# Kernel optimization log

Measured on AMD Instinct MI355X. Metric: run time of the kernel, lower is better.

## Reference

```python
import jax, jax.numpy as jnp
import numpy as np

L, H, NH, I = 12, 768, 12, 3072
DH = H // NH
EPS = 1e-12
STD = 0.02

def _ln(x, g, b):
    m = jnp.mean(x, axis=-1, keepdims=True)
    v = jnp.mean(jnp.square(x - m), axis=-1, keepdims=True)
    return (x - m) * jax.lax.rsqrt(v + EPS) * g + b

def setup_inputs() -> dict:
    key = jax.random.key(0)
    ks = jax.random.split(key, 6)
    return {
        "hidden_states": jax.random.normal(ks[0], (8, 512, H), dtype=jnp.float32),
        "attention_mask": jnp.zeros((8, 1, 1, 512), dtype=jnp.float32),
        "normA_gamma": jnp.ones((L, H), jnp.float32),
        "normA_beta": jnp.zeros((L, H), jnp.float32),
        "normB_gamma": jnp.ones((L, H), jnp.float32),
        "normB_beta": jnp.zeros((L, H), jnp.float32),
        "wa": jax.random.normal(ks[1], (L, 3 * H, H), jnp.float32) * STD,
        "ba": jnp.zeros((L, 3 * H), jnp.float32),
        "wb": jax.random.normal(ks[2], (L, H, H), jnp.float32) * STD,
        "bb": jnp.zeros((L, H), jnp.float32),
        "wc": jax.random.normal(ks[3], (L, I, H), jnp.float32) * STD,
        "bc": jnp.zeros((L, I), jnp.float32),
        "wd": jax.random.normal(ks[4], (L, H, I), jnp.float32) * STD,
        "bd": jnp.zeros((L, H), jnp.float32),
    }

def _encoder(hidden_states, attention_mask, normA_gamma, normA_beta, normB_gamma,
             normB_beta, wa, ba, wb, bb, wc, bc, wd, bd):
    B, S, _ = hidden_states.shape
    scale = 1.0 / jnp.sqrt(jnp.float32(DH))

    def layer(x, p):
        ga, bA, gB, bB_, Wa, Ba, Wb, Bb, Wc, Bc, Wd, Bd = p
        # fused QKV: [B,S,3H]
        qkv = jnp.einsum('bsh,oh->bso', x, Wa) + Ba
        q, k, v = jnp.split(qkv, 3, axis=-1)
        q = q.reshape(B, S, NH, DH)
        k = k.reshape(B, S, NH, DH)
        v = v.reshape(B, S, NH, DH)
        scores = jnp.einsum('bqnd,bknd->bnqk', q, k) * scale + attention_mask
        probs = jax.nn.softmax(scores, axis=-1)
        ctx = jnp.einsum('bnqk,bknd->bqnd', probs, v).reshape(B, S, H)
        attn_out = jnp.einsum('bsh,oh->bso', ctx, Wb) + Bb
        x = _ln(x + attn_out, ga, bA)           # post-LN after attention
        h = jax.nn.gelu(jnp.einsum('bsh,ih->bsi', x, Wc) + Bc, approximate=False)
        ffn_out = jnp.einsum('bsi,hi->bsh', h, Wd) + Bd
        x = _ln(x + ffn_out, gB, bB_)           # post-LN after FFN
        return x, None

    params = (normA_gamma, normA_beta, normB_gamma, normB_beta,
              wa, ba, wb, bb, wc, bc, wd, bd)
    out, _ = jax.lax.scan(layer, hidden_states, params)
    return out

def reference(hidden_states, attention_mask, normA_gamma, normA_beta, normB_gamma,
              normB_beta, wa, ba, wb, bb, wc, bc, wd, bd):
    return _encoder(hidden_states, attention_mask, normA_gamma, normA_beta,
                    normB_gamma, normB_beta, wa, ba, wb, bb, wc, bc, wd, bd)
```

## Files before the change

kernel.cpp:

```cpp
#include <hip/hip_runtime.h>
#include <hip/hip_bf16.h>
#include <cmath>

typedef __bf16 bf16;
typedef __attribute__((ext_vector_type(8))) __bf16 bf16x8;
typedef __attribute__((ext_vector_type(4))) float f32x4;

#define DEV __device__ __forceinline__

constexpr int HDIM = 768, NHEADS = 12, DHEAD = 64, IDIM = 3072, BATCH = 8, SEQ = 512;
constexpr int MTOK = BATCH * SEQ;
constexpr int H3 = 3 * HDIM;
constexpr float SCALE = 0.125f;

DEV void gld16(const bf16* g, bf16* l) {
  __builtin_amdgcn_global_load_lds((const __attribute__((address_space(1))) void*)g,
                                   (__attribute__((address_space(3))) void*)l, 16, 0, 0);
}

__global__ void k_cvt_all(const float* __restrict__ a, const float* __restrict__ b,
                          const float* __restrict__ c, const float* __restrict__ d,
                          bf16* __restrict__ oa, bf16* __restrict__ ob,
                          bf16* __restrict__ oc, bf16* __restrict__ od,
                          long na, long nb, long nc, long nd) {
  long i0 = ((long)blockIdx.x * blockDim.x + threadIdx.x) * 4;
  long st = (long)gridDim.x * blockDim.x * 4;
  union U { bf16 t[4]; short4 s; };
  for (long i = i0; i < na; i += st) {
    float4 v = *(const float4*)(a + i);
    U u; u.t[0] = (bf16)v.x; u.t[1] = (bf16)v.y; u.t[2] = (bf16)v.z; u.t[3] = (bf16)v.w;
    *(short4*)(oa + i) = u.s;
  }
  for (long i = i0; i < nb; i += st) {
    float4 v = *(const float4*)(b + i);
    U u; u.t[0] = (bf16)v.x; u.t[1] = (bf16)v.y; u.t[2] = (bf16)v.z; u.t[3] = (bf16)v.w;
    *(short4*)(ob + i) = u.s;
  }
  for (long i = i0; i < nc; i += st) {
    float4 v = *(const float4*)(c + i);
    U u; u.t[0] = (bf16)v.x; u.t[1] = (bf16)v.y; u.t[2] = (bf16)v.z; u.t[3] = (bf16)v.w;
    *(short4*)(oc + i) = u.s;
  }
  for (long i = i0; i < nd; i += st) {
    float4 v = *(const float4*)(d + i);
    U u; u.t[0] = (bf16)v.x; u.t[1] = (bf16)v.y; u.t[2] = (bf16)v.z; u.t[3] = (bf16)v.w;
    *(short4*)(od + i) = u.s;
  }
}

__global__ void k_initx(const float* __restrict__ s, float* __restrict__ xf,
                        bf16* __restrict__ xb, int n4) {
  int i = blockIdx.x * blockDim.x + threadIdx.x;
  int st = gridDim.x * blockDim.x;
  for (; i < n4; i += st) {
    float4 v = ((const float4*)s)[i];
    ((float4*)xf)[i] = v;
    union { bf16 t[4]; short4 q; } u;
    u.t[0] = (bf16)v.x; u.t[1] = (bf16)v.y; u.t[2] = (bf16)v.z; u.t[3] = (bf16)v.w;
    ((short4*)xb)[i] = u.q;
  }
}

template <int OUT>
__global__ __launch_bounds__(256) void k_gemm(const bf16* __restrict__ A,
                                              const bf16* __restrict__ W,
                                              const float* __restrict__ bias,
                                              void* __restrict__ C,
                                              bf16* __restrict__ vt,
                                              int M, int N, int K) {
  __shared__ alignas(128) bf16 As[2][128 * 32];
  __shared__ alignas(128) bf16 Bs[2][128 * 32];
  const int tid = threadIdx.x;
  const int lane = tid & 63, wave = tid >> 6;
  const int wr = wave >> 1, wc = wave & 1;
  const int bx = blockIdx.x, by = blockIdx.y;
  const bf16* Ab = A + (size_t)by * 128 * K;
  const bf16* Bb = W + (size_t)bx * 128 * K;
  const int s0 = tid, s1 = tid + 256;
  const int r0 = s0 >> 2, c0 = ((s0 & 3) ^ ((r0 >> 1) & 3)) << 3;
  const int r1 = s1 >> 2, c1 = ((s1 & 3) ^ ((r1 >> 1) & 3)) << 3;

  f32x4 acc[4][4] = {};
  const int KT = K >> 5;
  int cur = 0;
  gld16(Ab + (size_t)r0 * K + c0, &As[0][s0 * 8]);
  gld16(Ab + (size_t)r1 * K + c1, &As[0][s1 * 8]);
  gld16(Bb + (size_t)r0 * K + c0, &Bs[0][s0 * 8]);
  gld16(Bb + (size_t)r1 * K + c1, &Bs[0][s1 * 8]);

  const int r = lane & 15, kg = lane >> 4;
  for (int kt = 0; kt < KT; ++kt) {
    __syncthreads();
    if (kt + 1 < KT) {
      int k0 = (kt + 1) << 5;
      gld16(Ab + (size_t)r0 * K + k0 + c0, &As[cur ^ 1][s0 * 8]);
      gld16(Ab + (size_t)r1 * K + k0 + c1, &As[cur ^ 1][s1 * 8]);
      gld16(Bb + (size_t)r0 * K + k0 + c0, &Bs[cur ^ 1][s0 * 8]);
      gld16(Bb + (size_t)r1 * K + k0 + c1, &Bs[cur ^ 1][s1 * 8]);
    }
    const bf16* Ac = As[cur];
    const bf16* Bc = Bs[cur];
    bf16x8 af[4], bfr[4];
#pragma unroll
    for (int m = 0; m < 4; ++m) {
      int row = wr * 64 + m * 16 + r;
      af[m] = *(const bf16x8*)(Ac + row * 32 + ((kg ^ ((row >> 1) & 3)) << 3));
    }
#pragma unroll
    for (int n = 0; n < 4; ++n) {
      int row = wc * 64 + n * 16 + r;
      bfr[n] = *(const bf16x8*)(Bc + row * 32 + ((kg ^ ((row >> 1) & 3)) << 3));
    }
#pragma unroll
    for (int m = 0; m < 4; ++m)
#pragma unroll
      for (int n = 0; n < 4; ++n)
        acc[m][n] = __builtin_amdgcn_mfma_f32_16x16x32_bf16(af[m], bfr[n], acc[m][n], 0, 0, 0);
    cur ^= 1;
  }
  const int g = lane >> 4, c16 = lane & 15;
#pragma unroll
  for (int m = 0; m < 4; ++m) {
#pragma unroll
    for (int n = 0; n < 4; ++n) {
      int col = bx * 128 + wc * 64 + n * 16 + c16;
      float bv = bias[col];
      if (OUT == 3 && col >= 2 * HDIM) {
        int hh = (col - 2 * HDIM) >> 6, dd = (col - 2 * HDIM) & 63;
        int row0 = by * 128 + wr * 64 + m * 16 + g * 4;
        int bb_ = row0 >> 9, ss = row0 & 511;
        union { bf16 t[4]; short4 q; } u;
#pragma unroll
        for (int j = 0; j < 4; ++j) u.t[j] = (bf16)(acc[m][n][j] + bv);
        *(short4*)(vt + (((size_t)(bb_ * NHEADS + hh) * DHEAD + dd) * SEQ + ss)) = u.q;
      } else {
#pragma unroll
        for (int j = 0; j < 4; ++j) {
          int row = by * 128 + wr * 64 + m * 16 + g * 4 + j;
          float v = acc[m][n][j] + bv;
          if (OUT == 2) v = 0.5f * v * (1.0f + erff(v * 0.70710678118f));
          ((bf16*)C)[(size_t)row * N + col] = (bf16)v;
        }
      }
    }
  }
}

__global__ __launch_bounds__(256) void k_gemm_sk(const bf16* __restrict__ A,
                                                 const bf16* __restrict__ W,
                                                 bf16* __restrict__ C,
                                                 int M, int N, int Kc, int ld) {
  __shared__ alignas(128) bf16 As[2][128 * 32];
  __shared__ alignas(128) bf16 Bs[2][128 * 32];
  const int tid = threadIdx.x;
  const int lane = tid & 63, wave = tid >> 6;
  const int wr = wave >> 1, wc = wave & 1;
  const int bx = blockIdx.x, by = blockIdx.y, kz = blockIdx.z;
  const bf16* Ab = A + (size_t)by * 128 * ld + (size_t)kz * Kc;
  const bf16* Bb = W + (size_t)bx * 128 * ld + (size_t)kz * Kc;
  bf16* Cz = C + (size_t)kz * M * N;
  const int s0 = tid, s1 = tid + 256;
  const int r0 = s0 >> 2, c0 = ((s0 & 3) ^ ((r0 >> 1) & 3)) << 3;
  const int r1 = s1 >> 2, c1 = ((s1 & 3) ^ ((r1 >> 1) & 3)) << 3;

  f32x4 acc[4][4] = {};
  const int KT = Kc >> 5;
  int cur = 0;
  gld16(Ab + (size_t)r0 * ld + c0, &As[0][s0 * 8]);
  gld16(Ab + (size_t)r1 * ld + c1, &As[0][s1 * 8]);
  gld16(Bb + (size_t)r0 * ld + c0, &Bs[0][s0 * 8]);
  gld16(Bb + (size_t)r1 * ld + c1, &Bs[0][s1 * 8]);

  const int r = lane & 15, kg = lane >> 4;
  for (int kt = 0; kt < KT; ++kt) {
    __syncthreads();
    if (kt + 1 < KT) {
      int k0 = (kt + 1) << 5;
      gld16(Ab + (size_t)r0 * ld + k0 + c0, &As[cur ^ 1][s0 * 8]);
      gld16(Ab + (size_t)r1 * ld + k0 + c1, &As[cur ^ 1][s1 * 8]);
      gld16(Bb + (size_t)r0 * ld + k0 + c0, &Bs[cur ^ 1][s0 * 8]);
      gld16(Bb + (size_t)r1 * ld + k0 + c1, &Bs[cur ^ 1][s1 * 8]);
    }
    const bf16* Ac = As[cur];
    const bf16* Bc = Bs[cur];
    bf16x8 af[4], bfr[4];
#pragma unroll
    for (int m = 0; m < 4; ++m) {
      int row = wr * 64 + m * 16 + r;
      af[m] = *(const bf16x8*)(Ac + row * 32 + ((kg ^ ((row >> 1) & 3)) << 3));
    }
#pragma unroll
    for (int n = 0; n < 4; ++n) {
      int row = wc * 64 + n * 16 + r;
      bfr[n] = *(const bf16x8*)(Bc + row * 32 + ((kg ^ ((row >> 1) & 3)) << 3));
    }
#pragma unroll
    for (int m = 0; m < 4; ++m)
#pragma unroll
      for (int n = 0; n < 4; ++n)
        acc[m][n] = __builtin_amdgcn_mfma_f32_16x16x32_bf16(af[m], bfr[n], acc[m][n], 0, 0, 0);
    cur ^= 1;
  }
  const int g = lane >> 4, c16 = lane & 15;
#pragma unroll
  for (int m = 0; m < 4; ++m)
#pragma unroll
    for (int n = 0; n < 4; ++n) {
      int col = bx * 128 + wc * 64 + n * 16 + c16;
#pragma unroll
      for (int j = 0; j < 4; ++j) {
        int row = by * 128 + wr * 64 + m * 16 + g * 4 + j;
        Cz[(size_t)row * N + col] = (bf16)acc[m][n][j];
      }
    }
}

__global__ __launch_bounds__(256) void k_attn(const bf16* __restrict__ qkv,
                                              const bf16* __restrict__ vT,
                                              const float* __restrict__ mask,
                                              bf16* __restrict__ ctx) {
  __shared__ alignas(128) bf16 smem[20480];
  bf16* Qs = smem;
  bf16* Ks = smem + 4096;
  bf16* Vs = smem;
  bf16* Ps = smem + 16384;
  const int tid = threadIdx.x, lane = tid & 63, wave = tid >> 6;
  const int q0 = blockIdx.x * 64;
  const int h = blockIdx.y, b = blockIdx.z;
  const int bh = b * NHEADS + h;
  const bf16* qbase = qkv + (size_t)(b * SEQ) * H3 + h * DHEAD;
  const bf16* kbase = qbase + HDIM;
  const bf16* Vsrc = vT + (size_t)bh * DHEAD * SEQ;
  const int r15 = lane & 15, kg = lane >> 4;

  for (int s = tid; s < 512; s += 256) {
    int r = s >> 3, sl = s & 7;
    gld16(qbase + (size_t)(q0 + r) * H3 + ((sl ^ (r & 7)) << 3), &Qs[s * 8]);
  }
  f32x4 acc[32];
#pragma unroll
  for (int f = 0; f < 32; ++f) acc[f] = (f32x4){0.f, 0.f, 0.f, 0.f};

  for (int half = 0; half < 2; ++half) {
    for (int s = tid; s < 2048; s += 256) {
      int r = s >> 3, sl = s & 7;
      gld16(kbase + (size_t)(half * 256 + r) * H3 + ((sl ^ (r & 7)) << 3), &Ks[s * 8]);
    }
    __syncthreads();
#pragma unroll
    for (int ks = 0; ks < 2; ++ks) {
      int qrow = wave * 16 + r15;
      int sl = ks * 4 + kg;
      bf16x8 aq = *(const bf16x8*)(Qs + qrow * 64 + ((sl ^ (qrow & 7)) << 3));
#pragma unroll
      for (int nf = 0; nf < 16; ++nf) {
        int krow = nf * 16 + r15;
        bf16x8 bk = *(const bf16x8*)(Ks + krow * 64 + ((sl ^ (krow & 7)) << 3));
        acc[half * 16 + nf] =
            __builtin_amdgcn_mfma_f32_16x16x32_bf16(aq, bk, acc[half * 16 + nf], 0, 0, 0);
      }
    }
    __syncthreads();
  }

#pragma unroll
  for (int i = 0; i < 8; ++i) {
    int g16 = tid + i * 256;
    int d = g16 >> 5, c = g16 & 31;
    gld16(Vsrc + (size_t)d * SEQ + ((c ^ (d & 7)) << 3), &Vs[g16 * 8]);
  }

  const float* mrow = mask + b * SEQ;
#pragma unroll
  for (int f = 0; f < 32; ++f) {
    float mv = mrow[f * 16 + r15];
#pragma unroll
    for (int j = 0; j < 4; ++j) acc[f][j] = acc[f][j] * SCALE + mv;
  }
#pragma unroll
  for (int j = 0; j < 4; ++j) {
    float m = -1e30f;
#pragma unroll
    for (int f = 0; f < 32; ++f) m = fmaxf(m, acc[f][j]);
    m = fmaxf(m, __shfl_xor(m, 1));
    m = fmaxf(m, __shfl_xor(m, 2));
    m = fmaxf(m, __shfl_xor(m, 4));
    m = fmaxf(m, __shfl_xor(m, 8));
    float sum = 0.f;
#pragma unroll
    for (int f = 0; f < 32; ++f) { acc[f][j] = __expf(acc[f][j] - m); sum += acc[f][j]; }
    sum += __shfl_xor(sum, 1);
    sum += __shfl_xor(sum, 2);
    sum += __shfl_xor(sum, 4);
    sum += __shfl_xor(sum, 8);
    float inv = 1.0f / sum;
#pragma unroll
    for (int f = 0; f < 32; ++f) acc[f][j] *= inv;
  }
  __syncthreads();

  f32x4 pvacc[4] = {};
  bf16* Pw = Ps + wave * (16 * 32);
#pragma unroll
  for (int half = 0; half < 2; ++half) {
    if (half == 1) {
      __syncthreads();
#pragma unroll
      for (int i = 0; i < 8; ++i) {
        int g16 = tid + i * 256;
        int d = g16 >> 5, c = g16 & 31;
        gld16(Vsrc + (size_t)d * SEQ + 256 + ((c ^ (d & 7)) << 3), &Vs[g16 * 8]);
      }
      __syncthreads();
    }
#pragma unroll
    for (int kc8 = 0; kc8 < 8; ++kc8) {
      int kc = half * 8 + kc8;
#pragma unroll
      for (int fb = 0; fb < 2; ++fb)
#pragma unroll
        for (int j = 0; j < 4; ++j) {
          int q = kg * 4 + j, k = fb * 16 + r15;
          Pw[q * 32 + ((((k >> 3) ^ ((q >> 1) & 3)) << 3) | (k & 7))] =
              (bf16)acc[kc * 2 + fb][j];
        }
      bf16x8 pa = *(const bf16x8*)(Pw + r15 * 32 + ((kg ^ ((r15 >> 1) & 3)) << 3));
#pragma unroll
      for (int n = 0; n < 4; ++n) {
        int d = n * 16 + r15;
        bf16x8 vb = *(const bf16x8*)(Vs + d * 256 + (((kc8 * 4 + kg) ^ (d & 7)) << 3));
        pvacc[n] = __builtin_amdgcn_mfma_f32_16x16x32_bf16(pa, vb, pvacc[n], 0, 0, 0);
      }
    }
  }

  bf16* crow = ctx + (size_t)(b * SEQ + q0 + wave * 16) * HDIM + h * DHEAD;
#pragma unroll
  for (int n = 0; n < 4; ++n)
#pragma unroll
    for (int j = 0; j < 4; ++j)
      crow[(size_t)(kg * 4 + j) * HDIM + n * 16 + r15] = (bf16)pvacc[n][j];
}

__global__ __launch_bounds__(256) void k_ln4(const float* __restrict__ x,
                                             const bf16* __restrict__ d,
                                             const float* __restrict__ bias,
                                             const float* __restrict__ gamma,
                                             const float* __restrict__ beta,
                                             float* __restrict__ xo, bf16* __restrict__ xb) {
  const size_t MH = (size_t)MTOK * HDIM;
  int row = blockIdx.x;
  const float* xr = x + (size_t)row * HDIM;
  const bf16* dr = d + (size_t)row * HDIM;
  int t = threadIdx.x;
  float v[3];
  float s1 = 0.f, s2 = 0.f;
#pragma unroll
  for (int i = 0; i < 3; ++i) {
    int c = i * 256 + t;
    float a = xr[c] + bias[c] + (float)dr[c] + (float)dr[c + MH] +
              (float)dr[c + 2 * MH] + (float)dr[c + 3 * MH];
    v[i] = a; s1 += a; s2 += a * a;
  }
#pragma unroll
  for (int o = 32; o; o >>= 1) { s1 += __shfl_down(s1, o); s2 += __shfl_down(s2, o); }
  __shared__ float red[8];
  int wv = t >> 6, lane = t & 63;
  if (lane == 0) { red[wv] = s1; red[4 + wv] = s2; }
  __syncthreads();
  s1 = red[0] + red[1] + red[2] + red[3];
  s2 = red[4] + red[5] + red[6] + red[7];
  float mean = s1 * (1.0f / 768.0f);
  float var = s2 * (1.0f / 768.0f) - mean * mean;
  float rs = rsqrtf(var + 1e-12f);
  float* xro = xo + (size_t)row * HDIM;
  bf16* xbr = xb + (size_t)row * HDIM;
#pragma unroll
  for (int i = 0; i < 3; ++i) {
    int c = i * 256 + t;
    float o = (v[i] - mean) * rs * gamma[c] + beta[c];
    xro[c] = o; xbr[c] = (bf16)o;
  }
}

extern "C" void kernel_launch(void* const* d_in, const int* in_sizes, int n_in,
                              void* d_out, int out_size, void* d_ws, size_t ws_size,
                              hipStream_t stream) {
  const float* hidden = (const float*)d_in[0];
  const float* mask   = (const float*)d_in[1];
  const float* nAg    = (const float*)d_in[2];
  const float* nAb    = (const float*)d_in[3];
  const float* nBg    = (const float*)d_in[4];
  const float* nBb    = (const float*)d_in[5];
  const float* wa     = (const float*)d_in[6];
  const float* ba     = (const float*)d_in[7];
  const float* wb     = (const float*)d_in[8];
  const float* bb     = (const float*)d_in[9];
  const float* wc     = (const float*)d_in[10];
  const float* bc     = (const float*)d_in[11];
  const float* wd     = (const float*)d_in[12];
  const float* bd     = (const float*)d_in[13];

  char* p = (char*)d_ws;
  auto alloc = [&](size_t bytes) {
    char* r = p;
    p += (bytes + 255) & ~(size_t)255;
    return (void*)r;
  };
  float* xf   = (float*)alloc((size_t)MTOK * HDIM * 4);
  bf16* xb    = (bf16*)alloc((size_t)MTOK * HDIM * 2);
  bf16* qkv   = (bf16*)alloc((size_t)MTOK * H3 * 2);
  bf16* vT    = (bf16*)alloc((size_t)BATCH * NHEADS * DHEAD * SEQ * 2);
  bf16* ctx   = (bf16*)alloc((size_t)MTOK * HDIM * 2);
  bf16* hbuf  = (bf16*)alloc((size_t)MTOK * IDIM * 2);
  bf16* dres  = (bf16*)alloc((size_t)4 * MTOK * HDIM * 2);

  const size_t wa_n = (size_t)12 * H3 * HDIM;
  const size_t wb_n = (size_t)12 * HDIM * HDIM;
  const size_t wc_n = (size_t)12 * IDIM * HDIM;
  const size_t wd_n = (size_t)12 * HDIM * IDIM;
  size_t used = (size_t)(p - (char*)d_ws);
  const bool upfront = ws_size >= used + (wa_n + wb_n + wc_n + wd_n) * 2 + 8192;

  bf16* wab = (bf16*)alloc((upfront ? wa_n : (size_t)H3 * HDIM) * 2);
  bf16* wbb = (bf16*)alloc((upfront ? wb_n : (size_t)HDIM * HDIM) * 2);
  bf16* wcb = (bf16*)alloc((upfront ? wc_n : (size_t)IDIM * HDIM) * 2);
  bf16* wdb = (bf16*)alloc((upfront ? wd_n : (size_t)HDIM * IDIM) * 2);

  k_initx<<<1024, 256, 0, stream>>>(hidden, xf, xb, MTOK * HDIM / 4);
  if (upfront)
    k_cvt_all<<<2048, 256, 0, stream>>>(wa, wb, wc, wd, wab, wbb, wcb, wdb,
                                        (long)wa_n, (long)wb_n, (long)wc_n, (long)wd_n);

  for (int l = 0; l < 12; ++l) {
    bf16* waL = upfront ? wab + (size_t)l * H3 * HDIM : wab;
    bf16* wbL = upfront ? wbb + (size_t)l * HDIM * HDIM : wbb;
    bf16* wcL = upfront ? wcb + (size_t)l * IDIM * HDIM : wcb;
    bf16* wdL = upfront ? wdb + (size_t)l * HDIM * IDIM : wdb;
    if (!upfront)
      k_cvt_all<<<2048, 256, 0, stream>>>(
          wa + (size_t)l * H3 * HDIM, wb + (size_t)l * HDIM * HDIM,
          wc + (size_t)l * IDIM * HDIM, wd + (size_t)l * HDIM * IDIM,
          waL, wbL, wcL, wdL,
          (long)H3 * HDIM, (long)HDIM * HDIM, (long)IDIM * HDIM, (long)HDIM * IDIM);

    k_gemm<3><<<dim3(H3 / 128, MTOK / 128), 256, 0, stream>>>(
        xb, waL, ba + (size_t)l * H3, qkv, vT, MTOK, H3, HDIM);
    k_attn<<<dim3(SEQ / 64, NHEADS, BATCH), 256, 0, stream>>>(qkv, vT, mask, ctx);
    k_gemm_sk<<<dim3(HDIM / 128, MTOK / 128, 4), 256, 0, stream>>>(
        ctx, wbL, dres, MTOK, HDIM, HDIM / 4, HDIM);
    k_ln4<<<MTOK, 256, 0, stream>>>(xf, dres, bb + (size_t)l * HDIM,
                                    nAg + (size_t)l * HDIM, nAb + (size_t)l * HDIM, xf, xb);
    k_gemm<2><<<dim3(IDIM / 128, MTOK / 128), 256, 0, stream>>>(
        xb, wcL, bc + (size_t)l * IDIM, hbuf, nullptr, MTOK, IDIM, HDIM);
    k_gemm_sk<<<dim3(HDIM / 128, MTOK / 128, 4), 256, 0, stream>>>(
        hbuf, wdL, dres, MTOK, HDIM, IDIM / 4, IDIM);
    float* xout = (l == 11) ? (float*)d_out : xf;
    k_ln4<<<MTOK, 256, 0, stream>>>(xf, dres, bd + (size_t)l * HDIM,
                                    nBg + (size_t)l * HDIM, nBb + (size_t)l * HDIM, xout, xb);
  }
}
```

Baseline: 2.145 ms.

## Keep residual stream in bf16 and vectorize layernorm and conversion kernels

Removes the fp32 copy of the hidden state, so the residual stream is read from and written to bf16 only, with fp32 output written just on the last layer. The layernorm kernel now uses 192 threads each handling 4 contiguous elements with vector loads and stores. The weight conversion kernel is split into per-tensor launches that process 8 elements per iteration. This cuts memory traffic in the layernorm steps, but rounding the residual to bf16 every layer adds accuracy risk.

Result: faster. 2.067 ms (-3.7%).

```diff
diff --git a/kernel.cpp b/kernel.cpp
--- a/kernel.cpp
+++ b/kernel.cpp
@@ -5,6 +5,7 @@
 typedef __bf16 bf16;
 typedef __attribute__((ext_vector_type(8))) __bf16 bf16x8;
 typedef __attribute__((ext_vector_type(4))) float f32x4;
+typedef __attribute__((ext_vector_type(8))) short s16x8;
 
 #define DEV __device__ __forceinline__
 
@@ -18,46 +19,29 @@
                                    (__attribute__((address_space(3))) void*)l, 16, 0, 0);
 }
 
-__global__ void k_cvt_all(const float* __restrict__ a, const float* __restrict__ b,
-                          const float* __restrict__ c, const float* __restrict__ d,
-                          bf16* __restrict__ oa, bf16* __restrict__ ob,
-                          bf16* __restrict__ oc, bf16* __restrict__ od,
-                          long na, long nb, long nc, long nd) {
-  long i0 = ((long)blockIdx.x * blockDim.x + threadIdx.x) * 4;
-  long st = (long)gridDim.x * blockDim.x * 4;
-  union U { bf16 t[4]; short4 s; };
-  for (long i = i0; i < na; i += st) {
-    float4 v = *(const float4*)(a + i);
-    U u; u.t[0] = (bf16)v.x; u.t[1] = (bf16)v.y; u.t[2] = (bf16)v.z; u.t[3] = (bf16)v.w;
-    *(short4*)(oa + i) = u.s;
-  }
-  for (long i = i0; i < nb; i += st) {
-    float4 v = *(const float4*)(b + i);
-    U u; u.t[0] = (bf16)v.x; u.t[1] = (bf16)v.y; u.t[2] = (bf16)v.z; u.t[3] = (bf16)v.w;
-    *(short4*)(ob + i) = u.s;
-  }
-  for (long i = i0; i < nc; i += st) {
-    float4 v = *(const float4*)(c + i);
-    U u; u.t[0] = (bf16)v.x; u.t[1] = (bf16)v.y; u.t[2] = (bf16)v.z; u.t[3] = (bf16)v.w;
-    *(short4*)(oc + i) = u.s;
-  }
-  for (long i = i0; i < nd; i += st) {
-    float4 v = *(const float4*)(d + i);
-    U u; u.t[0] = (bf16)v.x; u.t[1] = (bf16)v.y; u.t[2] = (bf16)v.z; u.t[3] = (bf16)v.w;
-    *(short4*)(od + i) = u.s;
-  }
-}
-
-__global__ void k_initx(const float* __restrict__ s, float* __restrict__ xf,
-                        bf16* __restrict__ xb, int n4) {
-  int i = blockIdx.x * blockDim.x + threadIdx.x;
-  int st = gridDim.x * blockDim.x;
-  for (; i < n4; i += st) {
-    float4 v = ((const float4*)s)[i];
-    ((float4*)xf)[i] = v;
-    union { bf16 t[4]; short4 q; } u;
-    u.t[0] = (bf16)v.x; u.t[1] = (bf16)v.y; u.t[2] = (bf16)v.z; u.t[3] = (bf16)v.w;
-    ((short4*)xb)[i] = u.q;
+__global__ void k_cvt(const float* __restrict__ s, bf16* __restrict__ o, long n8) {
+  long i = (long)blockIdx.x * blockDim.x + threadIdx.x;
+  long st = (long)gridDim.x * blockDim.x;
+  for (; i < n8; i += st) {
+    const float4* p = (const float4*)s + i * 2;
+    float4 v0 = p[0], v1 = p[1];
+    union { bf16 t[8]; s16x8 v; } u;
+    u.t[0] = (bf16)v0.x; u.t[1] = (bf16)v0.y; u.t[2] = (bf16)v0.z; u.t[3] = (bf16)v0.w;
+    u.t[4] = (bf16)v1.x; u.t[5] = (bf16)v1.y; u.t[6] = (bf16)v1.z; u.t[7] = (bf16)v1.w;
+    *(s16x8*)(o + i * 8) = u.v;
+  }
+}
+
+__global__ void k_init_xb(const float* __restrict__ s, bf16* __restrict__ xb, long n8) {
+  long i = (long)blockIdx.x * blockDim.x + threadIdx.x;
+  long st = (long)gridDim.x * blockDim.x;
+  for (; i < n8; i += st) {
+    const float4* p = (const float4*)s + i * 2;
+    float4 v0 = p[0], v1 = p[1];
+    union { bf16 t[8]; s16x8 v; } u;
+    u.t[0] = (bf16)v0.x; u.t[1] = (bf16)v0.y; u.t[2] = (bf16)v0.z; u.t[3] = (bf16)v0.w;
+    u.t[4] = (bf16)v1.x; u.t[5] = (bf16)v1.y; u.t[6] = (bf16)v1.z; u.t[7] = (bf16)v1.w;
+    *(s16x8*)(xb + i * 8) = u.v;
   }
 }
 
@@ -342,44 +326,58 @@
       crow[(size_t)(kg * 4 + j) * HDIM + n * 16 + r15] = (bf16)pvacc[n][j];
 }
 
-__global__ __launch_bounds__(256) void k_ln4(const float* __restrict__ x,
+__global__ __launch_bounds__(192) void k_ln4(const bf16* __restrict__ x,
                                              const bf16* __restrict__ d,
                                              const float* __restrict__ bias,
                                              const float* __restrict__ gamma,
                                              const float* __restrict__ beta,
-                                             float* __restrict__ xo, bf16* __restrict__ xb) {
+                                             bf16* __restrict__ xo, float* __restrict__ fo) {
   const size_t MH = (size_t)MTOK * HDIM;
   int row = blockIdx.x;
-  const float* xr = x + (size_t)row * HDIM;
+  int t = threadIdx.x;
+  int c = t * 4;
+  const bf16* xr = x + (size_t)row * HDIM;
   const bf16* dr = d + (size_t)row * HDIM;
-  int t = threadIdx.x;
-  float v[3];
+  union S4 { bf16 t[4]; short4 s; };
+  S4 xv, d0, d1, d2, d3;
+  xv.s = *(const short4*)(xr + c);
+  d0.s = *(const short4*)(dr + c);
+  d1.s = *(const short4*)(dr + MH + c);
+  d2.s = *(const short4*)(dr + 2 * MH + c);
+  d3.s = *(const short4*)(dr + 3 * MH + c);
+  float4 bv = *(const float4*)(bias + c);
+  float a[4];
   float s1 = 0.f, s2 = 0.f;
 #pragma unroll
-  for (int i = 0; i < 3; ++i) {
-    int c = i * 256 + t;
-    float a = xr[c] + bias[c] + (float)dr[c] + (float)dr[c + MH] +
-              (float)dr[c + 2 * MH] + (float)dr[c + 3 * MH];
-    v[i] = a; s1 += a; s2 += a * a;
+  for (int j = 0; j < 4; ++j) {
+    float b_ = (j == 0) ? bv.x : (j == 1) ? bv.y : (j == 2) ? bv.z : bv.w;
+    a[j] = (float)xv.t[j] + b_ + (float)d0.t[j] + (float)d1.t[j] + (float)d2.t[j] +
+           (float)d3.t[j];
+    s1 += a[j]; s2 += a[j] * a[j];
   }
 #pragma unroll
   for (int o = 32; o; o >>= 1) { s1 += __shfl_down(s1, o); s2 += __shfl_down(s2, o); }
-  __shared__ float red[8];
+  __shared__ float red[6];
   int wv = t >> 6, lane = t & 63;
-  if (lane == 0) { red[wv] = s1; red[4 + wv] = s2; }
+  if (lane == 0) { red[wv] = s1; red[3 + wv] = s2; }
   __syncthreads();
-  s1 = red[0] + red[1] + red[2] + red[3];
-  s2 = red[4] + red[5] + red[6] + red[7];
+  s1 = red[0] + red[1] + red[2];
+  s2 = red[3] + red[4] + red[5];
   float mean = s1 * (1.0f / 768.0f);
   float var = s2 * (1.0f / 768.0f) - mean * mean;
   float rs = rsqrtf(var + 1e-12f);
-  float* xro = xo + (size_t)row * HDIM;
-  bf16* xbr = xb + (size_t)row * HDIM;
-#pragma unroll
-  for (int i = 0; i < 3; ++i) {
-    int c = i * 256 + t;
-    float o = (v[i] - mean) * rs * gamma[c] + beta[c];
-    xro[c] = o; xbr[c] = (bf16)o;
+  float4 gv = *(const float4*)(gamma + c);
+  float4 btv = *(const float4*)(beta + c);
+  float o0 = (a[0] - mean) * rs * gv.x + btv.x;
+  float o1 = (a[1] - mean) * rs * gv.y + btv.y;
+  float o2 = (a[2] - mean) * rs * gv.z + btv.z;
+  float o3 = (a[3] - mean) * rs * gv.w + btv.w;
+  S4 ov;
+  ov.t[0] = (bf16)o0; ov.t[1] = (bf16)o1; ov.t[2] = (bf16)o2; ov.t[3] = (bf16)o3;
+  *(short4*)(xo + (size_t)row * HDIM + c) = ov.s;
+  if (fo) {
+    float4 f4 = {o0, o1, o2, o3};
+    *(float4*)(fo + (size_t)row * HDIM + c) = f4;
   }
 }
 
@@ -407,7 +405,6 @@
     p += (bytes + 255) & ~(size_t)255;
     return (void*)r;
   };
-  float* xf   = (float*)alloc((size_t)MTOK * HDIM * 4);
   bf16* xb    = (bf16*)alloc((size_t)MTOK * HDIM * 2);
   bf16* qkv   = (bf16*)alloc((size_t)MTOK * H3 * 2);
   bf16* vT    = (bf16*)alloc((size_t)BATCH * NHEADS * DHEAD * SEQ * 2);
@@ -427,36 +424,40 @@
   bf16* wcb = (bf16*)alloc((upfront ? wc_n : (size_t)IDIM * HDIM) * 2);
   bf16* wdb = (bf16*)alloc((upfront ? wd_n : (size_t)HDIM * IDIM) * 2);
 
-  k_initx<<<1024, 256, 0, stream>>>(hidden, xf, xb, MTOK * HDIM / 4);
-  if (upfront)
-    k_cvt_all<<<2048, 256, 0, stream>>>(wa, wb, wc, wd, wab, wbb, wcb, wdb,
-                                        (long)wa_n, (long)wb_n, (long)wc_n, (long)wd_n);
+  k_init_xb<<<1024, 256, 0, stream>>>(hidden, xb, (long)MTOK * HDIM / 8);
+  if (upfront) {
+    k_cvt<<<2048, 256, 0, stream>>>(wa, wab, (long)(wa_n / 8));
+    k_cvt<<<2048, 256, 0, stream>>>(wb, wbb, (long)(wb_n / 8));
+    k_cvt<<<2048, 256, 0, stream>>>(wc, wcb, (long)(wc_n / 8));
+    k_cvt<<<2048, 256, 0, stream>>>(wd, wdb, (long)(wd_n / 8));
+  }
 
   for (int l = 0; l < 12; ++l) {
     bf16* waL = upfront ? wab + (size_t)l * H3 * HDIM : wab;
     bf16* wbL = upfront ? wbb + (size_t)l * HDIM * HDIM : wbb;
     bf16* wcL = upfront ? wcb + (size_t)l * IDIM * HDIM : wcb;
     bf16* wdL = upfront ? wdb + (size_t)l * HDIM * IDIM : wdb;
-    if (!upfront)
-      k_cvt_all<<<2048, 256, 0, stream>>>(
-          wa + (size_t)l * H3 * HDIM, wb + (size_t)l * HDIM * HDIM,
-          wc + (size_t)l * IDIM * HDIM, wd + (size_t)l * HDIM * IDIM,
-          waL, wbL, wcL, wdL,
-          (long)H3 * HDIM, (long)HDIM * HDIM, (long)IDIM * HDIM, (long)HDIM * IDIM);
+    if (!upfront) {
+      k_cvt<<<2048, 256, 0, stream>>>(wa + (size_t)l * H3 * HDIM, waL, (long)(H3 * HDIM / 8));
+      k_cvt<<<2048, 256, 0, stream>>>(wb + (size_t)l * HDIM * HDIM, wbL, (long)(HDIM * HDIM / 8));
+      k_cvt<<<2048, 256, 0, stream>>>(wc + (size_t)l * IDIM * HDIM, wcL, (long)(IDIM * HDIM / 8));
+      k_cvt<<<2048, 256, 0, stream>>>(wd + (size_t)l * HDIM * IDIM, wdL, (long)(HDIM * IDIM / 8));
+    }
 
     k_gemm<3><<<dim3(H3 / 128, MTOK / 128), 256, 0, stream>>>(
         xb, waL, ba + (size_t)l * H3, qkv, vT, MTOK, H3, HDIM);
     k_attn<<<dim3(SEQ / 64, NHEADS, BATCH), 256, 0, stream>>>(qkv, vT, mask, ctx);
     k_gemm_sk<<<dim3(HDIM / 128, MTOK / 128, 4), 256, 0, stream>>>(
         ctx, wbL, dres, MTOK, HDIM, HDIM / 4, HDIM);
-    k_ln4<<<MTOK, 256, 0, stream>>>(xf, dres, bb + (size_t)l * HDIM,
-                                    nAg + (size_t)l * HDIM, nAb + (size_t)l * HDIM, xf, xb);
+    k_ln4<<<MTOK, 192, 0, stream>>>(xb, dres, bb + (size_t)l * HDIM,
+                                    nAg + (size_t)l * HDIM, nAb + (size_t)l * HDIM,
+                                    xb, nullptr);
     k_gemm<2><<<dim3(IDIM / 128, MTOK / 128), 256, 0, stream>>>(
         xb, wcL, bc + (size_t)l * IDIM, hbuf, nullptr, MTOK, IDIM, HDIM);
     k_gemm_sk<<<dim3(HDIM / 128, MTOK / 128, 4), 256, 0, stream>>>(
         hbuf, wdL, dres, MTOK, HDIM, IDIM / 4, IDIM);
-    float* xout = (l == 11) ? (float*)d_out : xf;
-    k_ln4<<<MTOK, 256, 0, stream>>>(xf, dres, bd + (size_t)l * HDIM,
-                                    nBg + (size_t)l * HDIM, nBb + (size_t)l * HDIM, xout, xb);
-  }
-}
+    k_ln4<<<MTOK, 192, 0, stream>>>(xb, dres, bd + (size_t)l * HDIM,
+                                    nBg + (size_t)l * HDIM, nBb + (size_t)l * HDIM,
+                                    xb, (l == 11) ? (float*)d_out : nullptr);
+  }
+}
```
